# Optimization experiments

Hardware: AMD Instinct MI355X
Metric: run time of the kernel (lower is better)

The kernel has to match this reference:

```python
import jax, jax.numpy as jnp
import numpy as np

B, S, HID = 2, 2048, 4096
NH, NKV, HD = 32, 8, 128
G = 128  # quant group size along input dim
NEG_INF = -1e9


def _rope_tables(key):
    inv_freq = 1.0 / (10000.0 ** (jnp.arange(0, HD, 2, dtype=jnp.float32) / HD))  # [HD/2]
    pos = jnp.arange(S, dtype=jnp.float32)
    ang = pos[:, None] * inv_freq[None, :]                  # [S, HD/2]
    emb = jnp.concatenate([ang, ang], axis=-1)              # [S, HD]
    cos = jnp.broadcast_to(jnp.cos(emb)[None], (B, S, HD))
    sin = jnp.broadcast_to(jnp.sin(emb)[None], (B, S, HD))
    return cos, sin


def setup_inputs() -> dict:
    key = jax.random.key(0)
    ks = jax.random.split(key, 10)
    hidden_states = jax.random.normal(ks[0], (B, S, HID), dtype=jnp.float32)
    cos, sin = _rope_tables(ks[1])
    causal = jnp.tril(jnp.ones((S, S), dtype=bool))
    attention_mask = jnp.broadcast_to(
        jnp.where(causal, 0.0, NEG_INF).astype(jnp.float32)[None, None], (B, 1, S, S))

    def qlinear(k, out_dim, in_dim):
        k1, k2 = jax.random.split(k)
        qw = jax.random.randint(k1, (out_dim, in_dim), 0, 16, dtype=jnp.int32)
        scale = jax.random.uniform(k2, (out_dim, in_dim // G), dtype=jnp.float32) * 0.01 + 0.001
        return qw, scale

    q_qw, q_scale = qlinear(ks[2], NH * HD, HID)
    k_qw, k_scale = qlinear(ks[3], NKV * HD, HID)
    v_qw, v_scale = qlinear(ks[4], NKV * HD, HID)
    o_qw, o_scale = qlinear(ks[5], HID, NH * HD)
    return dict(hidden_states=hidden_states, cos=cos, sin=sin,
                attention_mask=attention_mask,
                q_qw=q_qw, q_scale=q_scale, k_qw=k_qw, k_scale=k_scale,
                v_qw=v_qw, v_scale=v_scale, o_qw=o_qw, o_scale=o_scale)


def _dequant(qw, scale):
    # int4 codes in [0,16), zero-point 8, per-(row, input-group) scale
    out_dim, in_dim = qw.shape
    w = (qw.astype(jnp.float32) - 8.0).reshape(out_dim, in_dim // G, G)
    return (w * scale[:, :, None]).reshape(out_dim, in_dim)


def _rotate_half(x):
    x1, x2 = jnp.split(x, 2, axis=-1)
    return jnp.concatenate([-x2, x1], axis=-1)


def reference(hidden_states, cos, sin, attention_mask,
              q_qw, q_scale, k_qw, k_scale, v_qw, v_scale, o_qw, o_scale):
    scaling = HD ** -0.5
    Wq = _dequant(q_qw, q_scale)
    Wk = _dequant(k_qw, k_scale)
    Wv = _dequant(v_qw, v_scale)
    Wo = _dequant(o_qw, o_scale)

    q = jnp.einsum('bsh,oh->bso', hidden_states, Wq).reshape(B, S, NH, HD).transpose(0, 2, 1, 3)
    k = jnp.einsum('bsh,oh->bso', hidden_states, Wk).reshape(B, S, NKV, HD).transpose(0, 2, 1, 3)
    v = jnp.einsum('bsh,oh->bso', hidden_states, Wv).reshape(B, S, NKV, HD).transpose(0, 2, 1, 3)

    c = cos[:, None, :, :]  # [B,1,S,HD]
    s = sin[:, None, :, :]
    q = q * c + _rotate_half(q) * s
    k = k * c + _rotate_half(k) * s

    groups = NH // NKV
    k = jnp.repeat(k, groups, axis=1)  # [B,NH,S,HD]
    v = jnp.repeat(v, groups, axis=1)

    scores = jnp.einsum('bhsd,bhtd->bhst', q, k) * scaling + attention_mask
    probs = jax.nn.softmax(scores, axis=-1)
    ctx = jnp.einsum('bhst,bhtd->bhsd', probs, v)        # [B,NH,S,HD]
    ctx = ctx.transpose(0, 2, 1, 3).reshape(B, S, NH * HD)
    return jnp.einsum('bso,ho->bsh', ctx, Wo.T) if False else jnp.einsum('bsi,oi->bso', ctx, Wo)
```

## Files before the change

### kernel.cpp

```cpp
#include <hip/hip_runtime.h>
#include <hip/hip_bf16.h>

#define B_ 2
#define S_ 2048
#define HID_ 4096
#define NH_ 32
#define NKV_ 8
#define HD_ 128
#define T_ (B_*S_)

typedef __bf16 bf16;
typedef __bf16 bf16x8 __attribute__((ext_vector_type(8)));
typedef __bf16 bf16x4 __attribute__((ext_vector_type(4)));
typedef float f32x4 __attribute__((ext_vector_type(4)));

__device__ __forceinline__ void load_lds16(const void* g, void* l) {
  __builtin_amdgcn_global_load_lds((const __attribute__((address_space(1))) void*)g,
                                   (__attribute__((address_space(3))) void*)l, 16, 0, 0);
}

#define DPP_ROR(x, n) __int_as_float(__builtin_amdgcn_update_dpp( \
    __float_as_int(x), __float_as_int(x), 0x120 | (n), 0xf, 0xf, false))
__device__ __forceinline__ float red16_max(float x) {
  x = fmaxf(x, DPP_ROR(x, 1)); x = fmaxf(x, DPP_ROR(x, 2));
  x = fmaxf(x, DPP_ROR(x, 4)); x = fmaxf(x, DPP_ROR(x, 8));
  return x;
}
__device__ __forceinline__ float red16_sum(float x) {
  x += DPP_ROR(x, 1); x += DPP_ROR(x, 2);
  x += DPP_ROR(x, 4); x += DPP_ROR(x, 8);
  return x;
}

__global__ __launch_bounds__(256) void cvt_bf16_kernel(const float* __restrict__ in,
                                                       bf16* __restrict__ out, int n4) {
  int idx = blockIdx.x * 256 + threadIdx.x;
  if (idx >= n4) return;
  float4 v = ((const float4*)in)[idx];
  bf16x4 o;
  o.x = (bf16)v.x; o.y = (bf16)v.y; o.z = (bf16)v.z; o.w = (bf16)v.w;
  ((bf16x4*)out)[idx] = o;
}

__global__ __launch_bounds__(256) void dequant_kernel(const int* __restrict__ qw,
                                                      const float* __restrict__ scale,
                                                      bf16* __restrict__ out,
                                                      int OD, int ID) {
  int idx = blockIdx.x * 256 + threadIdx.x;
  int perRow = ID >> 3;
  int total = OD * perRow;
  if (idx >= total) return;
  int o = idx / perRow;
  int ic = idx - o * perRow;
  float s = scale[o * (ID >> 7) + ((ic * 8) >> 7)];
  const int* q = qw + (size_t)o * ID + ic * 8;
  int4 q0 = *(const int4*)q;
  int4 q1 = *(const int4*)(q + 4);
  bf16x8 r;
  r[0] = (bf16)((q0.x - 8) * s);
  r[1] = (bf16)((q0.y - 8) * s);
  r[2] = (bf16)((q0.z - 8) * s);
  r[3] = (bf16)((q0.w - 8) * s);
  r[4] = (bf16)((q1.x - 8) * s);
  r[5] = (bf16)((q1.y - 8) * s);
  r[6] = (bf16)((q1.z - 8) * s);
  r[7] = (bf16)((q1.w - 8) * s);
  *(bf16x8*)(out + (size_t)o * ID + ic * 8) = r;
}

__global__ __launch_bounds__(256) void gemm_bt_kernel(const bf16* __restrict__ A,
                                                      const bf16* __restrict__ Bm,
                                                      void* __restrict__ Cout,
                                                      int N, int K, int c_fp32) {
  __shared__ bf16 As[8192];
  __shared__ bf16 Bs[8192];
  int tid = threadIdx.x;
  int wave = tid >> 6, lane = tid & 63, quad = lane >> 4, l16 = lane & 15;
  int m0 = blockIdx.y * 128, n0 = blockIdx.x * 128;
  int wm = (wave >> 1) * 64, wn = (wave & 1) * 64;

  int srow = lane >> 3;
  int schunk = (lane & 7) ^ (srow & 7);
  const bf16* Ab[4];
  const bf16* Bb[4];
#pragma unroll
  for (int u = 0; u < 4; u++) {
    int t = wave + 4 * u;
    Ab[u] = A  + (size_t)(m0 + 8 * t + srow) * K + schunk * 8;
    Bb[u] = Bm + (size_t)(n0 + 8 * t + srow) * K + schunk * 8;
  }

  f32x4 acc[4][4];
#pragma unroll
  for (int mt = 0; mt < 4; mt++)
#pragma unroll
    for (int nt = 0; nt < 4; nt++) acc[mt][nt] = (f32x4){0.f, 0.f, 0.f, 0.f};

  for (int k0 = 0; k0 < K; k0 += 64) {
    __syncthreads();
#pragma unroll
    for (int u = 0; u < 4; u++) {
      int t = wave + 4 * u;
      load_lds16(Ab[u] + k0, (char*)As + t * 1024);
      load_lds16(Bb[u] + k0, (char*)Bs + t * 1024);
    }
    __syncthreads();
#pragma unroll
    for (int kk = 0; kk < 2; kk++) {
      bf16x8 af[4], bfr[4];
#pragma unroll
      for (int mt = 0; mt < 4; mt++) {
        int r = wm + mt * 16 + l16;
        af[mt] = *(const bf16x8*)((const char*)As + r * 128 + (((kk * 4 + quad) ^ (r & 7)) << 4));
      }
#pragma unroll
      for (int nt = 0; nt < 4; nt++) {
        int r = wn + nt * 16 + l16;
        bfr[nt] = *(const bf16x8*)((const char*)Bs + r * 128 + (((kk * 4 + quad) ^ (r & 7)) << 4));
      }
#pragma unroll
      for (int mt = 0; mt < 4; mt++)
#pragma unroll
        for (int nt = 0; nt < 4; nt++)
          acc[mt][nt] = __builtin_amdgcn_mfma_f32_16x16x32_bf16(af[mt], bfr[nt], acc[mt][nt], 0, 0, 0);
    }
  }

#pragma unroll
  for (int mt = 0; mt < 4; mt++)
#pragma unroll
    for (int nt = 0; nt < 4; nt++)
#pragma unroll
      for (int r = 0; r < 4; r++) {
        int rr = m0 + wm + mt * 16 + quad * 4 + r;
        int cc = n0 + wn + nt * 16 + l16;
        if (c_fp32) ((float*)Cout)[(size_t)rr * N + cc] = acc[mt][nt][r];
        else        ((bf16*)Cout)[(size_t)rr * N + cc] = (bf16)acc[mt][nt][r];
      }
}

__global__ __launch_bounds__(256) void gemm_rope_kernel(const bf16* __restrict__ A,
                                                        const bf16* __restrict__ Bm,
                                                        bf16* __restrict__ Out,
                                                        int N, int K,
                                                        const float* __restrict__ cosT,
                                                        const float* __restrict__ sinT,
                                                        float outscale) {
  __shared__ char smem[32768];
  bf16* As = (bf16*)smem;
  bf16* Bs = (bf16*)(smem + 16384);
  float* Ex = (float*)smem;
  int tid = threadIdx.x;
  int wave = tid >> 6, lane = tid & 63, quad = lane >> 4, l16 = lane & 15;
  int m0 = blockIdx.y * 128, n0 = blockIdx.x * 128;
  int wm = (wave >> 1) * 64, wn = (wave & 1) * 64;

  int srow = lane >> 3;
  int schunk = (lane & 7) ^ (srow & 7);
  const bf16* Ab[4];
  const bf16* Bb[4];
#pragma unroll
  for (int u = 0; u < 4; u++) {
    int t = wave + 4 * u;
    Ab[u] = A  + (size_t)(m0 + 8 * t + srow) * K + schunk * 8;
    Bb[u] = Bm + (size_t)(n0 + 8 * t + srow) * K + schunk * 8;
  }

  f32x4 acc[4][4];
#pragma unroll
  for (int mt = 0; mt < 4; mt++)
#pragma unroll
    for (int nt = 0; nt < 4; nt++) acc[mt][nt] = (f32x4){0.f, 0.f, 0.f, 0.f};

  for (int k0 = 0; k0 < K; k0 += 64) {
    __syncthreads();
#pragma unroll
    for (int u = 0; u < 4; u++) {
      int t = wave + 4 * u;
      load_lds16(Ab[u] + k0, (char*)As + t * 1024);
      load_lds16(Bb[u] + k0, (char*)Bs + t * 1024);
    }
    __syncthreads();
#pragma unroll
    for (int kk = 0; kk < 2; kk++) {
      bf16x8 af[4], bfr[4];
#pragma unroll
      for (int mt = 0; mt < 4; mt++) {
        int r = wm + mt * 16 + l16;
        af[mt] = *(const bf16x8*)((const char*)As + r * 128 + (((kk * 4 + quad) ^ (r & 7)) << 4));
      }
#pragma unroll
      for (int nt = 0; nt < 4; nt++) {
        int r = wn + nt * 16 + l16;
        bfr[nt] = *(const bf16x8*)((const char*)Bs + r * 128 + (((kk * 4 + quad) ^ (r & 7)) << 4));
      }
#pragma unroll
      for (int mt = 0; mt < 4; mt++)
#pragma unroll
        for (int nt = 0; nt < 4; nt++)
          acc[mt][nt] = __builtin_amdgcn_mfma_f32_16x16x32_bf16(af[mt], bfr[nt], acc[mt][nt], 0, 0, 0);
    }
  }

  int myb = tid * 17;
  int pb = (tid ^ 64) * 17;
#pragma unroll
  for (int mt = 0; mt < 4; mt++) {
    __syncthreads();
#pragma unroll
    for (int nt = 0; nt < 4; nt++)
#pragma unroll
      for (int r = 0; r < 4; r++)
        Ex[myb + nt * 4 + r] = acc[mt][nt][r];
    __syncthreads();
    int rowb = m0 + wm + mt * 16 + quad * 4;
#pragma unroll
    for (int nt = 0; nt < 4; nt++) {
      int cc = n0 + wn + nt * 16 + l16;
      int d = cc & 127;
#pragma unroll
      for (int r = 0; r < 4; r++) {
        int row = rowb + r;
        int t = row & (S_ - 1);
        float self = acc[mt][nt][r];
        float other = Ex[pb + nt * 4 + r];
        float c = cosT[t * 128 + d], s = sinT[t * 128 + d];
        float o = (d < 64) ? (self * c - other * s) : (self * c + other * s);
        Out[(size_t)row * N + cc] = (bf16)(o * outscale);
      }
    }
  }
}

__global__ __launch_bounds__(512, 4) void attn_kernel(const bf16* __restrict__ Qm,
                                                      const bf16* __restrict__ Km,
                                                      const bf16* __restrict__ VtG,
                                                      bf16* __restrict__ Cm) {
  __shared__ char sK[32768];
  __shared__ char sV[16384];
  __shared__ char sP[16384];
  int tid = threadIdx.x;
  int wave = tid >> 6, lane = tid & 63, quad = lane >> 4, l16 = lane & 15;
  int h = blockIdx.y, b = blockIdx.z;
  int kvh = h >> 2;

  const bf16* Kb[2];
  const bf16* Vb[2];
  {
    int r4 = lane >> 4, c16 = lane & 15;
    int r8 = lane >> 3, c8 = lane & 7;
#pragma unroll
    for (int u = 0; u < 2; u++) {
      int t = wave * 2 + u;
      int key = 4 * t + r4;
      int kc = c16 ^ (key & 7);
      Kb[u] = Km + (size_t)(b * S_ + key) * (NKV_ * HD_) + kvh * HD_ + kc * 8;
      int d = 8 * t + r8;
      int vc = c8 ^ (d & 7);
      Vb[u] = VtG + (size_t)(kvh * HD_ + d) * T_ + (size_t)b * S_ + vc * 8;
    }
  }

  for (int pass = 0; pass < 2; pass++) {
    int qt = pass ? ((S_ / 128 - 1) - (int)blockIdx.x) : (int)blockIdx.x;
    int q0 = qt * 128;
    int jend = q0 + 128;

#pragma unroll
    for (int u = 0; u < 2; u++)
      load_lds16(Kb[u], sK + (wave * 2 + u) * 1024);

    bf16x8 aQ[4];
    {
      int row = q0 + wave * 16 + l16;
      const bf16* qb = Qm + (size_t)(b * S_ + row) * (NH_ * HD_) + h * HD_;
#pragma unroll
      for (int kt = 0; kt < 4; kt++)
        aQ[kt] = *(const bf16x8*)(qb + kt * 32 + quad * 8);
    }

    float mcur[4], lcur[4];
    f32x4 O[8];
#pragma unroll
    for (int r = 0; r < 4; r++) { mcur[r] = -1e30f; lcur[r] = 0.f; }
#pragma unroll
    for (int n = 0; n < 8; n++) O[n] = (f32x4){0.f, 0.f, 0.f, 0.f};

    for (int j0 = 0; j0 < jend; j0 += 64) {
      int cur = (j0 >> 6) & 1;
      __syncthreads();
      if (j0 + 64 < jend) {
#pragma unroll
        for (int u = 0; u < 2; u++)
          load_lds16(Kb[u] + (size_t)(j0 + 64) * (NKV_ * HD_),
                     sK + (1 - cur) * 16384 + (wave * 2 + u) * 1024);
      }
#pragma unroll
      for (int u = 0; u < 2; u++)
        load_lds16(Vb[u] + j0, sV + (wave * 2 + u) * 1024);

      const char* Kc = sK + cur * 16384;
      f32x4 sc[4];
#pragma unroll
      for (int nt = 0; nt < 4; nt++) sc[nt] = (f32x4){0.f, 0.f, 0.f, 0.f};
#pragma unroll
      for (int kt = 0; kt < 4; kt++) {
        bf16x8 bk[4];
#pragma unroll
        for (int nt = 0; nt < 4; nt++) {
          int key = nt * 16 + l16;
          bk[nt] = *(const bf16x8*)(Kc + key * 256 + (((kt * 4 + quad) ^ (key & 7)) << 4));
        }
#pragma unroll
        for (int nt = 0; nt < 4; nt++)
          sc[nt] = __builtin_amdgcn_mfma_f32_16x16x32_bf16(aQ[kt], bk[nt], sc[nt], 0, 0, 0);
      }

      int rowb = q0 + wave * 16 + quad * 4;
      if (j0 + 63 > q0 + wave * 16) {
#pragma unroll
        for (int nt = 0; nt < 4; nt++) {
          int col = j0 + nt * 16 + l16;
#pragma unroll
          for (int r = 0; r < 4; r++)
            if (col > rowb + r) sc[nt][r] = -1e9f;
        }
      }

      float rmax[4], alpha[4], rsum[4];
#pragma unroll
      for (int r = 0; r < 4; r++) {
        float v = fmaxf(fmaxf(sc[0][r], sc[1][r]), fmaxf(sc[2][r], sc[3][r]));
        rmax[r] = red16_max(v);
        float mnew = fmaxf(mcur[r], rmax[r]);
        alpha[r] = exp2f(mcur[r] - mnew);
        mcur[r] = mnew;
      }
#pragma unroll
      for (int nt = 0; nt < 4; nt++)
#pragma unroll
        for (int r = 0; r < 4; r++)
          sc[nt][r] = exp2f(sc[nt][r] - mcur[r]);
#pragma unroll
      for (int r = 0; r < 4; r++) {
        float s = (sc[0][r] + sc[1][r]) + (sc[2][r] + sc[3][r]);
        rsum[r] = red16_sum(s);
        lcur[r] = lcur[r] * alpha[r] + rsum[r];
      }
#pragma unroll
      for (int n = 0; n < 8; n++)
#pragma unroll
        for (int r = 0; r < 4; r++) O[n][r] *= alpha[r];

      char* Pw = sP + wave * 2048;
#pragma unroll
      for (int nt = 0; nt < 4; nt++) {
        int key = nt * 16 + l16;
#pragma unroll
        for (int r = 0; r < 4; r++) {
          int m = quad * 4 + r;
          *(bf16*)(Pw + m * 128 + (((key >> 3) ^ (m & 7)) << 4) + (key & 7) * 2) =
              (bf16)sc[nt][r];
        }
      }

      __syncthreads();

#pragma unroll
      for (int kt = 0; kt < 2; kt++) {
        bf16x8 ap = *(const bf16x8*)(Pw + l16 * 128 + (((kt * 4 + quad) ^ (l16 & 7)) << 4));
#pragma unroll
        for (int nt = 0; nt < 8; nt++) {
          int d = nt * 16 + l16;
          bf16x8 bv = *(const bf16x8*)(sV + d * 128 + (((kt * 4 + quad) ^ (d & 7)) << 4));
          O[nt] = __builtin_amdgcn_mfma_f32_16x16x32_bf16(ap, bv, O[nt], 0, 0, 0);
        }
      }
    }

#pragma unroll
    for (int nt = 0; nt < 8; nt++)
#pragma unroll
      for (int r = 0; r < 4; r++) {
        int row = q0 + wave * 16 + quad * 4 + r;
        Cm[(size_t)(b * S_ + row) * (NH_ * HD_) + h * HD_ + nt * 16 + l16] =
            (bf16)(O[nt][r] / lcur[r]);
      }
  }
}

extern "C" void kernel_launch(void* const* d_in, const int* in_sizes, int n_in,
                              void* d_out, int out_size, void* d_ws, size_t ws_size,
                              hipStream_t stream) {
  const float* hidden = (const float*)d_in[0];
  const float* cosT   = (const float*)d_in[1];
  const float* sinT   = (const float*)d_in[2];
  const int*   q_qw = (const int*)d_in[4];
  const float* q_sc = (const float*)d_in[5];
  const int*   k_qw = (const int*)d_in[6];
  const float* k_sc = (const float*)d_in[7];
  const int*   v_qw = (const int*)d_in[8];
  const float* v_sc = (const float*)d_in[9];
  const int*   o_qw = (const int*)d_in[10];
  const float* o_sc = (const float*)d_in[11];

  const size_t MB = 1024 * 1024;
  char* ws = (char*)d_ws;
  bf16* Xb  = (bf16*)(ws);
  bf16* Wb  = (bf16*)(ws + 32 * MB);
  bf16* Qm  = (bf16*)(ws + 64 * MB);
  bf16* Km  = (bf16*)(ws + 96 * MB);
  bf16* VtG = (bf16*)(ws + 104 * MB);
  bf16* Cm  = Xb;

  cvt_bf16_kernel<<<(T_ * HID_ / 4 + 255) / 256, 256, 0, stream>>>(hidden, Xb, T_ * HID_ / 4);

  const float qscale = (float)(0.08838834764831845 * 1.4426950408889634);

  dequant_kernel<<<(4096 * 512 + 255) / 256, 256, 0, stream>>>(q_qw, q_sc, Wb, 4096, 4096);
  gemm_rope_kernel<<<dim3(32, 32), 256, 0, stream>>>(Xb, Wb, Qm, 4096, 4096, cosT, sinT, qscale);

  dequant_kernel<<<(1024 * 512 + 255) / 256, 256, 0, stream>>>(k_qw, k_sc, Wb, 1024, 4096);
  gemm_rope_kernel<<<dim3(8, 32), 256, 0, stream>>>(Xb, Wb, Km, 1024, 4096, cosT, sinT, 1.0f);

  dequant_kernel<<<(1024 * 512 + 255) / 256, 256, 0, stream>>>(v_qw, v_sc, Wb, 1024, 4096);
  gemm_bt_kernel<<<dim3(32, 8), 256, 0, stream>>>(Wb, Xb, VtG, 4096, 4096, 0);

  attn_kernel<<<dim3(8, NH_, B_), 512, 0, stream>>>(Qm, Km, VtG, Cm);

  dequant_kernel<<<(4096 * 512 + 255) / 256, 256, 0, stream>>>(o_qw, o_sc, Wb, 4096, 4096);
  gemm_bt_kernel<<<dim3(32, 32), 256, 0, stream>>>(Cm, Wb, d_out, 4096, 4096, 1);
}
```

Before: 900.1 us.

## Add 256x256-tile 8-wave GEMM with split-phase LDS pipelining for Q and O projections

Adds a new GEMM kernel that uses 256x256 output tiles with 512 threads, a double-buffered 128KB LDS with direct global-to-LDS loads, swizzled LDS addressing, an XCD-aware block remap, and phase-split loads interleaved with MFMA bursts under raised priority. The Q projection (with fused RoPE) and the O projection now use it in place of the older 128-tile kernels. The intent is more data reuse per LDS byte and better overlap of memory traffic with matrix math on the two largest GEMMs. In exchange it brings heavy register and LDS pressure and only 256 workgroups, which may underfill the GPU.

Measured after the change: 829.1 us. 7.9% less time.

```diff
diff --git a/kernel.cpp b/kernel.cpp
--- a/kernel.cpp
+++ b/kernel.cpp
@@ -232,6 +232,165 @@
   }
 }
 
+template<int FUSE_ROPE, int C_FP32>
+__global__ __launch_bounds__(512, 2) void gemm256_kernel(const bf16* __restrict__ A,
+                                                         const bf16* __restrict__ Bm,
+                                                         void* __restrict__ Cout,
+                                                         int N, int K,
+                                                         const float* __restrict__ cosT,
+                                                         const float* __restrict__ sinT,
+                                                         float outscale) {
+  __shared__ char smem[131072];
+  const int tid = threadIdx.x;
+  const int wave = tid >> 6, lane = tid & 63, quad = lane >> 4, l16 = lane & 15;
+  const int wm = (wave >> 2) * 128, wn = (wave & 3) * 64;
+
+  int bid = blockIdx.y * gridDim.x + blockIdx.x;
+  int cpx = (gridDim.x * gridDim.y) >> 3;
+  int wgid = (bid & 7) * cpx + (bid >> 3);
+  int m0 = (wgid / gridDim.x) * 256;
+  int n0 = (wgid % gridDim.x) * 256;
+
+  const int srow = wave * 16 + (lane >> 2);
+  const int sc = (lane & 3) ^ ((lane >> 2) & 3) ^ quad;
+  const bf16* aS0 = A  + (size_t)(m0 + srow) * K + sc * 8;
+  const bf16* aS1 = A  + (size_t)(m0 + 128 + srow) * K + sc * 8;
+  const bf16* bS0 = Bm + (size_t)(n0 + srow) * K + sc * 8;
+  const bf16* bS1 = Bm + (size_t)(n0 + 128 + srow) * K + sc * 8;
+  const int wl = wave * 1024;
+
+  const int rslot = ((quad ^ (l16 & 3) ^ ((l16 >> 2) & 3)) << 4);
+  const int aoff = (wm + l16) * 64 + rslot;
+  const int boff = (wn + l16) * 64 + rslot;
+
+  f32x4 acc[8][4];
+#pragma unroll
+  for (int mt = 0; mt < 8; mt++)
+#pragma unroll
+    for (int nt = 0; nt < 4; nt++) acc[mt][nt] = (f32x4){0.f, 0.f, 0.f, 0.f};
+
+  load_lds16(aS0,      smem +     0 + wl); load_lds16(aS1,      smem +  8192 + wl);
+  load_lds16(bS0,      smem + 32768 + wl); load_lds16(bS1,      smem + 40960 + wl);
+  load_lds16(aS0 + 32, smem + 16384 + wl); load_lds16(aS1 + 32, smem + 24576 + wl);
+  load_lds16(bS0 + 32, smem + 49152 + wl); load_lds16(bS1 + 32, smem + 57344 + wl);
+  asm volatile("s_waitcnt vmcnt(0)" ::: "memory");
+  __builtin_amdgcn_s_barrier();
+
+  const int NT = K >> 6;
+  for (int t = 0; t < NT; ++t) {
+    const char* base = smem + (t & 1) * 65536;
+    char* nb = smem + ((t & 1) ^ 1) * 65536;
+    const int off = (t + 1) << 6;
+    const bool more = (t + 1) < NT;
+    bf16x8 afA[4], afB[4], bfr[4];
+
+#pragma unroll
+    for (int i = 0; i < 4; i++) afA[i] = *(const bf16x8*)(base + aoff + i * 1024);
+#pragma unroll
+    for (int i = 0; i < 4; i++) bfr[i] = *(const bf16x8*)(base + 32768 + boff + i * 1024);
+    if (more) { load_lds16(aS0 + off, nb + wl); load_lds16(aS1 + off, nb + 8192 + wl); }
+    __builtin_amdgcn_s_barrier();
+    __builtin_amdgcn_s_setprio(1);
+#pragma unroll
+    for (int mt = 0; mt < 4; mt++)
+#pragma unroll
+      for (int nt = 0; nt < 4; nt++)
+        acc[mt][nt] = __builtin_amdgcn_mfma_f32_16x16x32_bf16(afA[mt], bfr[nt], acc[mt][nt], 0, 0, 0);
+    __builtin_amdgcn_s_setprio(0);
+    __builtin_amdgcn_s_barrier();
+
+#pragma unroll
+    for (int i = 0; i < 4; i++) afB[i] = *(const bf16x8*)(base + aoff + (i + 4) * 1024);
+    if (more) { load_lds16(bS0 + off, nb + 32768 + wl); load_lds16(bS1 + off, nb + 40960 + wl); }
+    if (t == NT - 1) asm volatile("s_waitcnt vmcnt(0)" ::: "memory");
+    else             asm volatile("s_waitcnt vmcnt(4)" ::: "memory");
+    __builtin_amdgcn_s_barrier();
+    __builtin_amdgcn_s_setprio(1);
+#pragma unroll
+    for (int mt = 0; mt < 4; mt++)
+#pragma unroll
+      for (int nt = 0; nt < 4; nt++)
+        acc[mt + 4][nt] = __builtin_amdgcn_mfma_f32_16x16x32_bf16(afB[mt], bfr[nt], acc[mt + 4][nt], 0, 0, 0);
+    __builtin_amdgcn_s_setprio(0);
+    __builtin_amdgcn_s_barrier();
+
+#pragma unroll
+    for (int i = 0; i < 4; i++) afA[i] = *(const bf16x8*)(base + 16384 + aoff + i * 1024);
+#pragma unroll
+    for (int i = 0; i < 4; i++) bfr[i] = *(const bf16x8*)(base + 49152 + boff + i * 1024);
+    if (more) { load_lds16(aS0 + off + 32, nb + 16384 + wl); load_lds16(aS1 + off + 32, nb + 24576 + wl); }
+    __builtin_amdgcn_s_barrier();
+    __builtin_amdgcn_s_setprio(1);
+#pragma unroll
+    for (int mt = 0; mt < 4; mt++)
+#pragma unroll
+      for (int nt = 0; nt < 4; nt++)
+        acc[mt][nt] = __builtin_amdgcn_mfma_f32_16x16x32_bf16(afA[mt], bfr[nt], acc[mt][nt], 0, 0, 0);
+    __builtin_amdgcn_s_setprio(0);
+    __builtin_amdgcn_s_barrier();
+
+#pragma unroll
+    for (int i = 0; i < 4; i++) afB[i] = *(const bf16x8*)(base + 16384 + aoff + (i + 4) * 1024);
+    if (more) {
+      load_lds16(bS0 + off + 32, nb + 49152 + wl); load_lds16(bS1 + off + 32, nb + 57344 + wl);
+      asm volatile("s_waitcnt vmcnt(4)" ::: "memory");
+    }
+    __builtin_amdgcn_s_barrier();
+    __builtin_amdgcn_s_setprio(1);
+#pragma unroll
+    for (int mt = 0; mt < 4; mt++)
+#pragma unroll
+      for (int nt = 0; nt < 4; nt++)
+        acc[mt + 4][nt] = __builtin_amdgcn_mfma_f32_16x16x32_bf16(afB[mt], bfr[nt], acc[mt + 4][nt], 0, 0, 0);
+    __builtin_amdgcn_s_setprio(0);
+    __builtin_amdgcn_s_barrier();
+  }
+
+  if (FUSE_ROPE) {
+    float* Ex = (float*)smem;
+    int myb = tid * 17;
+    int pb = (tid ^ 64) * 17;
+#pragma unroll
+    for (int mt = 0; mt < 8; mt++) {
+      __syncthreads();
+#pragma unroll
+      for (int nt = 0; nt < 4; nt++)
+#pragma unroll
+        for (int r = 0; r < 4; r++)
+          Ex[myb + nt * 4 + r] = acc[mt][nt][r];
+      __syncthreads();
+      int rowb = m0 + wm + mt * 16 + quad * 4;
+#pragma unroll
+      for (int nt = 0; nt < 4; nt++) {
+        int cc = n0 + wn + nt * 16 + l16;
+        int d = cc & 127;
+#pragma unroll
+        for (int r = 0; r < 4; r++) {
+          int row = rowb + r;
+          int tp = row & (S_ - 1);
+          float self = acc[mt][nt][r];
+          float other = Ex[pb + nt * 4 + r];
+          float c = cosT[tp * 128 + d], s = sinT[tp * 128 + d];
+          float o = (d < 64) ? (self * c - other * s) : (self * c + other * s);
+          ((bf16*)Cout)[(size_t)row * N + cc] = (bf16)(o * outscale);
+        }
+      }
+    }
+  } else {
+#pragma unroll
+    for (int mt = 0; mt < 8; mt++)
+#pragma unroll
+      for (int nt = 0; nt < 4; nt++)
+#pragma unroll
+        for (int r = 0; r < 4; r++) {
+          int rr = m0 + wm + mt * 16 + quad * 4 + r;
+          int cc = n0 + wn + nt * 16 + l16;
+          if (C_FP32) ((float*)Cout)[(size_t)rr * N + cc] = acc[mt][nt][r];
+          else        ((bf16*)Cout)[(size_t)rr * N + cc] = (bf16)acc[mt][nt][r];
+        }
+  }
+}
+
 __global__ __launch_bounds__(512, 4) void attn_kernel(const bf16* __restrict__ Qm,
                                                       const bf16* __restrict__ Km,
                                                       const bf16* __restrict__ VtG,
@@ -418,7 +577,8 @@
   const float qscale = (float)(0.08838834764831845 * 1.4426950408889634);
 
   dequant_kernel<<<(4096 * 512 + 255) / 256, 256, 0, stream>>>(q_qw, q_sc, Wb, 4096, 4096);
-  gemm_rope_kernel<<<dim3(32, 32), 256, 0, stream>>>(Xb, Wb, Qm, 4096, 4096, cosT, sinT, qscale);
+  gemm256_kernel<1, 0><<<dim3(16, 16), 512, 0, stream>>>(Xb, Wb, Qm, 4096, 4096,
+                                                         cosT, sinT, qscale);
 
   dequant_kernel<<<(1024 * 512 + 255) / 256, 256, 0, stream>>>(k_qw, k_sc, Wb, 1024, 4096);
   gemm_rope_kernel<<<dim3(8, 32), 256, 0, stream>>>(Xb, Wb, Km, 1024, 4096, cosT, sinT, 1.0f);
@@ -429,5 +589,6 @@
   attn_kernel<<<dim3(8, NH_, B_), 512, 0, stream>>>(Qm, Km, VtG, Cm);
 
   dequant_kernel<<<(4096 * 512 + 255) / 256, 256, 0, stream>>>(o_qw, o_sc, Wb, 4096, 4096);
-  gemm_bt_kernel<<<dim3(32, 32), 256, 0, stream>>>(Cm, Wb, d_out, 4096, 4096, 1);
-}
+  gemm256_kernel<0, 1><<<dim3(16, 16), 512, 0, stream>>>(Cm, Wb, d_out, 4096, 4096,
+                                                         nullptr, nullptr, 1.0f);
+}
```
